# Kernel optimization log

Measured on AMD Instinct MI355X. Metric: run time of the kernel, lower is better.

## Reference

```python
import jax, jax.numpy as jnp
import numpy as np

N_NODES = 50000   # number of graph nodes
N_EDGES = 800000  # avg degree 16
D = 128           # in_dim == all hdims -> residual active every layer
L = 3             # len(cfg['hdims'])


def setup_inputs() -> dict:
    key = jax.random.key(0)
    ks = jax.random.split(key, 8)
    scale = 1.0 / np.sqrt(D)
    x = jax.random.normal(ks[0], (N_NODES, D), dtype=jnp.float32)
    edge_index = jax.random.randint(ks[1], (2, N_EDGES), 0, N_NODES, dtype=jnp.int32)
    in_fc_w = jax.random.normal(ks[2], (D, D), dtype=jnp.float32) * scale
    in_fc_b = jnp.zeros((D,), dtype=jnp.float32)
    # GraphConv per layer: lin_rel (with bias) applied to aggregated neighbors,
    # lin_root (no bias) applied to self features. All layers are DxD -> stack.
    w_rel = jax.random.normal(ks[3], (L, D, D), dtype=jnp.float32) * scale
    b_rel = jnp.zeros((L, D), dtype=jnp.float32)
    w_root = jax.random.normal(ks[4], (L, D, D), dtype=jnp.float32) * scale
    return {"x": x, "edge_index": edge_index, "in_fc_w": in_fc_w,
            "in_fc_b": in_fc_b, "w_rel": w_rel, "b_rel": b_rel, "w_root": w_root}


def reference(x, edge_index, in_fc_w, in_fc_b, w_rel, b_rel, w_root):
    src, dst = edge_index[0], edge_index[1]
    h = x @ in_fc_w + in_fc_b                     # in_fc
    for l in range(L):                            # fixed small layer count
        # GraphConv, aggr='add': gather source feats, scatter-add to targets
        agg = jax.ops.segment_sum(h[src], dst, num_segments=N_NODES)  # [N, D]
        out = agg @ w_rel[l] + b_rel[l] + h @ w_root[l]
        out = jax.nn.relu(out)
        h = out + h                               # residual (dims match)
    return h
```

## Files before the change

kernel.cpp:

```cpp
#include <hip/hip_runtime.h>
#include <hip/hip_bf16.h>


constexpr int D = 128;
constexpr int NB_SHIFT = 7;
constexpr int BCAP = 2560;
constexpr int CHUNK = 2048;

typedef __attribute__((ext_vector_type(8))) short bf16x8;
typedef __attribute__((ext_vector_type(4))) float f32x4;
typedef __attribute__((ext_vector_type(4))) unsigned int u32x4;

__device__ inline unsigned short f2bf(float f) {
    unsigned int u = __builtin_bit_cast(unsigned int, f);
    u += 0x7FFFu + ((u >> 16) & 1u);
    return (unsigned short)(u >> 16);
}
__device__ inline float bf2f(unsigned short v) {
    return __builtin_bit_cast(float, (unsigned int)v << 16);
}
__device__ inline float bf2f_lo(unsigned int v) {
    return __builtin_bit_cast(float, v << 16);
}
__device__ inline float bf2f_hi(unsigned int v) {
    return __builtin_bit_cast(float, v & 0xFFFF0000u);
}

__global__ __launch_bounds__(256) void prep(
    const float* __restrict__ x, const float* __restrict__ fc_w,
    const float* __restrict__ w_rel, const float* __restrict__ w_root,
    unsigned short* __restrict__ xb, unsigned short* __restrict__ Wp,
    int* __restrict__ cursor, int n4, int NB)
{
    int blk = blockIdx.x;
    const int nconv = (n4 + 255) / 256;
    if (blk < nconv) {
        int i = blk * 256 + threadIdx.x;
        if (i < n4) {
            float4 v = ((const float4*)x)[i];
            ushort4 o;
            o.x = f2bf(v.x); o.y = f2bf(v.y); o.z = f2bf(v.z); o.w = f2bf(v.w);
            ((ushort4*)xb)[i] = o;
        }
        return;
    }
    blk -= nconv;
    if (blk < 56) {
        int idx = blk * 256 + threadIdx.x;
        int mat  = idx >> 11;
        int rem  = idx & 2047;
        int tn   = rem >> 8;
        int ks   = (rem >> 6) & 3;
        int lane = rem & 63;
        const float* w = (mat == 0) ? fc_w
                       : (mat <= 3) ? w_rel  + (size_t)(mat - 1) * D * D
                                    : w_root + (size_t)(mat - 4) * D * D;
        unsigned short* wp = Wp + (size_t)mat * D * D + (size_t)rem * 8;
        int kbase = ks * 32 + (lane >> 4) * 8;
        int col   = tn * 16 + (lane & 15);
        #pragma unroll
        for (int j = 0; j < 8; ++j)
            wp[j] = f2bf(w[(size_t)(kbase + j) * D + col]);
        return;
    }
    blk -= 56;
    int i = blk * 256 + threadIdx.x;
    if (i < NB) cursor[i] = 0;
}

__global__ __launch_bounds__(256) void gemm_mfma(
    const unsigned short* __restrict__ A1, const unsigned short* __restrict__ W1p,
    const float* __restrict__ bias, unsigned short* __restrict__ hb_out, int N)
{
    const int tid  = threadIdx.x;
    const int wave = tid >> 6;
    const int lane = tid & 63;
    const int row0 = blockIdx.x * 64 + wave * 16;
    const int mrow = lane & 15;
    const int kgrp = lane >> 4;

    f32x4 acc[8];
    #pragma unroll
    for (int t = 0; t < 8; ++t) acc[t] = (f32x4){0.f, 0.f, 0.f, 0.f};

    int arow = row0 + mrow; if (arow >= N) arow = N - 1;
    const size_t abase = (size_t)arow * D + kgrp * 8;

    #pragma unroll
    for (int ks = 0; ks < 4; ++ks) {
        bf16x8 a1 = *(const bf16x8*)(A1 + abase + ks * 32);
        #pragma unroll
        for (int tn = 0; tn < 8; ++tn) {
            bf16x8 b = *(const bf16x8*)(W1p + ((size_t)((tn * 4 + ks) * 64 + lane) * 8));
            acc[tn] = __builtin_amdgcn_mfma_f32_16x16x32_bf16(a1, b, acc[tn], 0, 0, 0);
        }
    }

    const int r0 = row0 + kgrp * 4;
    #pragma unroll
    for (int tn = 0; tn < 8; ++tn) {
        const int col = tn * 16 + mrow;
        const float bv = bias[col];
        #pragma unroll
        for (int reg = 0; reg < 4; ++reg) {
            int r = r0 + reg;
            if (r < N) hb_out[(size_t)r * D + col] = f2bf(acc[tn][reg] + bv);
        }
    }
}

__global__ __launch_bounds__(256) void gemm_layer(
    const unsigned short* __restrict__ aggb, const unsigned short* __restrict__ hb_in,
    const unsigned short* __restrict__ Wrel, const unsigned short* __restrict__ Wroot,
    const float* __restrict__ bias,
    unsigned short* hb_out, float* out_f32, int N)
{
    const int tid  = threadIdx.x;
    const int wave = tid >> 6;
    const int lane = tid & 63;
    const int row0 = blockIdx.x * 64 + wave * 16;
    const int mrow = lane & 15;
    const int kgrp = lane >> 4;

    f32x4 acc[8];
    #pragma unroll
    for (int t = 0; t < 8; ++t) acc[t] = (f32x4){0.f, 0.f, 0.f, 0.f};

    int arow = row0 + mrow; if (arow >= N) arow = N - 1;
    const size_t abase = (size_t)arow * D + kgrp * 8;

    #pragma unroll
    for (int ks = 0; ks < 4; ++ks) {
        bf16x8 a1 = *(const bf16x8*)(aggb  + abase + ks * 32);
        bf16x8 a2 = *(const bf16x8*)(hb_in + abase + ks * 32);
        #pragma unroll
        for (int tn = 0; tn < 8; ++tn) {
            bf16x8 b1 = *(const bf16x8*)(Wrel  + ((size_t)((tn * 4 + ks) * 64 + lane) * 8));
            acc[tn] = __builtin_amdgcn_mfma_f32_16x16x32_bf16(a1, b1, acc[tn], 0, 0, 0);
            bf16x8 b2 = *(const bf16x8*)(Wroot + ((size_t)((tn * 4 + ks) * 64 + lane) * 8));
            acc[tn] = __builtin_amdgcn_mfma_f32_16x16x32_bf16(a2, b2, acc[tn], 0, 0, 0);
        }
    }

    const int r0 = row0 + kgrp * 4;
    #pragma unroll
    for (int tn = 0; tn < 8; ++tn) {
        const int col = tn * 16 + mrow;
        const float bv = bias[col];
        #pragma unroll
        for (int reg = 0; reg < 4; ++reg) {
            int r = r0 + reg;
            if (r < N) {
                float z = fmaxf(acc[tn][reg] + bv, 0.f);
                float o = z + bf2f(hb_in[(size_t)r * D + col]);
                if (out_f32 != nullptr) out_f32[(size_t)r * D + col] = o;
                else                    hb_out[(size_t)r * D + col] = f2bf(o);
            }
        }
    }
}

__global__ __launch_bounds__(256) void bucket_scatter(
    const int* __restrict__ src, const int* __restrict__ dst,
    unsigned int* __restrict__ entries, int* __restrict__ cursor, int E, int NB)
{
    __shared__ unsigned int   stage[CHUNK];
    __shared__ unsigned short bslot[CHUNK];
    __shared__ int lhist[512];
    __shared__ int lscan[512];
    __shared__ int lgbase[512];
    __shared__ int lcur[512];
    __shared__ int sh[256];

    const int base  = blockIdx.x * CHUNK;
    const int count = min(CHUNK, E - base);
    const int tid   = threadIdx.x;

    for (int i = tid; i < 512; i += 256) { lhist[i] = 0; lcur[i] = 0; }
    __syncthreads();

    for (int i = tid; i < count; i += 256)
        atomicAdd(&lhist[dst[base + i] >> NB_SHIFT], 1);
    __syncthreads();

    int v2 = lhist[2 * tid] + lhist[2 * tid + 1];
    sh[tid] = v2;
    __syncthreads();
    #pragma unroll
    for (int off = 1; off < 256; off <<= 1) {
        int t = (tid >= off) ? sh[tid - off] : 0;
        __syncthreads();
        sh[tid] += t;
        __syncthreads();
    }
    int excl2 = sh[tid] - v2;
    lscan[2 * tid]     = excl2;
    lscan[2 * tid + 1] = excl2 + lhist[2 * tid];
    __syncthreads();

    for (int t = tid; t < 512; t += 256) {
        int c = (t < NB) ? lhist[t] : 0;
        lgbase[t] = (c > 0) ? atomicAdd(&cursor[t], c) : 0;
    }
    __syncthreads();

    for (int i = tid; i < count; i += 256) {
        int d = dst[base + i];
        int s = src[base + i];
        int b = d >> NB_SHIFT;
        int p = atomicAdd(&lcur[b], 1);
        int slot = lscan[b] + p;
        stage[slot] = ((unsigned int)(d & ((1 << NB_SHIFT) - 1)) << 16) | (unsigned int)s;
        bslot[slot] = (unsigned short)b;
    }
    __syncthreads();

    for (int i = tid; i < count; i += 256) {
        int b   = bslot[i];
        int off = i - lscan[b] + lgbase[b];
        if (off < BCAP) entries[(size_t)b * BCAP + off] = stage[i];
    }
}

__global__ __launch_bounds__(256) void bucket_sort(
    const unsigned int* __restrict__ entries, const int* __restrict__ cursor,
    unsigned short* __restrict__ sorted_src, int* __restrict__ rs4,
    int N, int NB, float inv_range)
{
    const int b   = blockIdx.x;
    const int tid = threadIdx.x;

    __shared__ int nhist[512];
    __shared__ int nscan[512];
    __shared__ int ncur[512];
    __shared__ int sh[256];
    __shared__ unsigned short svals[BCAP];
    __shared__ int sgbase;

    int part = 0;
    for (int i = tid; i < b; i += 256) part += min(cursor[i], BCAP);
    sh[tid] = part;
    __syncthreads();
    for (int off = 128; off > 0; off >>= 1) {
        if (tid < off) sh[tid] += sh[tid + off];
        __syncthreads();
    }
    if (tid == 0) sgbase = sh[0];
    const int cnt = min(cursor[b], BCAP);
    __syncthreads();
    const int gbase = sgbase;

    for (int i = tid; i < 512; i += 256) { nhist[i] = 0; ncur[i] = 0; }
    __syncthreads();

    const unsigned int* ebase = entries + (size_t)b * BCAP;
    for (int i = tid; i < cnt; i += 256) {
        unsigned int e = ebase[i];
        int s = (int)(e & 0xFFFFu);
        int r = (int)((float)s * inv_range); if (r > 3) r = 3;
        atomicAdd(&nhist[(int)((e >> 16) << 2) | r], 1);
    }
    __syncthreads();

    int v2 = nhist[2 * tid] + nhist[2 * tid + 1];
    sh[tid] = v2;
    __syncthreads();
    #pragma unroll
    for (int off = 1; off < 256; off <<= 1) {
        int t = (tid >= off) ? sh[tid - off] : 0;
        __syncthreads();
        sh[tid] += t;
        __syncthreads();
    }
    int excl2 = sh[tid] - v2;
    nscan[2 * tid]     = excl2;
    nscan[2 * tid + 1] = excl2 + nhist[2 * tid];
    __syncthreads();

    for (int i = tid; i < 512; i += 256) {
        int n = (b << NB_SHIFT) + (i >> 2);
        if (n < N) rs4[(n << 2) + (i & 3)] = gbase + nscan[i];
    }
    if (b == NB - 1 && tid == 0) rs4[N << 2] = gbase + cnt;

    for (int i = tid; i < cnt; i += 256) {
        unsigned int e = ebase[i];
        int s = (int)(e & 0xFFFFu);
        int r = (int)((float)s * inv_range); if (r > 3) r = 3;
        int key = (int)((e >> 16) << 2) | r;
        int p = atomicAdd(&ncur[key], 1);
        svals[nscan[key] + p] = (unsigned short)s;
    }
    __syncthreads();

    unsigned short* obase = sorted_src + gbase;
    for (int i = tid; i < cnt; i += 256) obase[i] = svals[i];
}

__global__ __launch_bounds__(256) void aggregate_bf16(
    const unsigned short* __restrict__ hb, const int* __restrict__ rs4,
    const unsigned short* __restrict__ sorted_src, unsigned short* __restrict__ aggb, int N)
{
    const int tid  = threadIdx.x;
    const int wave = tid >> 6;
    const int lane = tid & 63;
    const int g    = lane >> 4;
    const int c    = lane & 15;
    const int n    = blockIdx.x * 16 + wave * 4 + g;
    if (n >= N) return;
    const int b = rs4[n << 2];
    const int e = rs4[(n << 2) + 4];

    float acc[8];
    #pragma unroll
    for (int q = 0; q < 8; ++q) acc[q] = 0.f;

    int j = b;
    for (; j + 4 <= e; j += 4) {
        int s0 = sorted_src[j];
        int s1 = sorted_src[j + 1];
        int s2 = sorted_src[j + 2];
        int s3 = sorted_src[j + 3];
        u32x4 v0 = *(const u32x4*)((const unsigned int*)(hb + (size_t)s0 * D) + c * 4);
        u32x4 v1 = *(const u32x4*)((const unsigned int*)(hb + (size_t)s1 * D) + c * 4);
        u32x4 v2 = *(const u32x4*)((const unsigned int*)(hb + (size_t)s2 * D) + c * 4);
        u32x4 v3 = *(const u32x4*)((const unsigned int*)(hb + (size_t)s3 * D) + c * 4);
        #pragma unroll
        for (int q = 0; q < 4; ++q) {
            acc[2 * q]     += (bf2f_lo(v0[q]) + bf2f_lo(v1[q])) + (bf2f_lo(v2[q]) + bf2f_lo(v3[q]));
            acc[2 * q + 1] += (bf2f_hi(v0[q]) + bf2f_hi(v1[q])) + (bf2f_hi(v2[q]) + bf2f_hi(v3[q]));
        }
    }
    for (; j < e; ++j) {
        int s = sorted_src[j];
        u32x4 v = *(const u32x4*)((const unsigned int*)(hb + (size_t)s * D) + c * 4);
        #pragma unroll
        for (int q = 0; q < 4; ++q) {
            acc[2 * q]     += bf2f_lo(v[q]);
            acc[2 * q + 1] += bf2f_hi(v[q]);
        }
    }

    u32x4 o;
    #pragma unroll
    for (int q = 0; q < 4; ++q)
        o[q] = (unsigned int)f2bf(acc[2 * q]) |
               ((unsigned int)f2bf(acc[2 * q + 1]) << 16);
    *(u32x4*)((unsigned int*)(aggb + (size_t)n * D) + c * 4) = o;
}

extern "C" void kernel_launch(void* const* d_in, const int* in_sizes, int n_in,
                              void* d_out, int out_size, void* d_ws, size_t ws_size,
                              hipStream_t stream)
{
    const float* x      = (const float*)d_in[0];
    const int*   ei     = (const int*)  d_in[1];
    const float* fc_w   = (const float*)d_in[2];
    const float* fc_b   = (const float*)d_in[3];
    const float* w_rel  = (const float*)d_in[4];
    const float* b_rel  = (const float*)d_in[5];
    const float* w_root = (const float*)d_in[6];
    float* out = (float*)d_out;

    const int N = in_sizes[0] / D;
    const int E = in_sizes[1] / 2;
    const int* src = ei;
    const int* dst = ei + E;
    const int NB = (N + (1 << NB_SHIFT) - 1) >> NB_SHIFT;

    char* p = (char*)d_ws;
    unsigned short* hb0  = (unsigned short*)p;  p += (size_t)N * D * sizeof(unsigned short);
    unsigned short* hb1  = (unsigned short*)p;  p += (size_t)N * D * sizeof(unsigned short);
    unsigned short* aggb = (unsigned short*)p;  p += (size_t)N * D * sizeof(unsigned short);
    unsigned short* Wp   = (unsigned short*)p;  p += (size_t)7 * D * D * sizeof(unsigned short);
    unsigned int* entries = (unsigned int*)p;   p += (size_t)NB * BCAP * sizeof(unsigned int);
    unsigned short* sorted_src = (unsigned short*)p;  p += (size_t)E * sizeof(unsigned short);
    int* rs4    = (int*)p;                      p += (size_t)(4 * N + 4) * sizeof(int);
    int* cursor = (int*)p;                      p += (size_t)NB * sizeof(int);

    unsigned short* Wp_in   = Wp;
    unsigned short* Wp_rel  = Wp + (size_t)1 * D * D;
    unsigned short* Wp_root = Wp + (size_t)4 * D * D;
    unsigned short* xb = aggb;

    const int n4 = N * D / 4;
    const int gemm_blocks = (N + 63) / 64;
    const int prep_blocks = (n4 + 255) / 256 + 56 + (NB + 255) / 256;

    prep<<<prep_blocks, 256, 0, stream>>>(x, fc_w, w_rel, w_root, xb, Wp, cursor, n4, NB);

    bucket_scatter<<<(E + CHUNK - 1) / CHUNK, 256, 0, stream>>>(
        src, dst, entries, cursor, E, NB);
    bucket_sort<<<NB, 256, 0, stream>>>(
        entries, cursor, sorted_src, rs4, N, NB, 4.0f / (float)N);

    gemm_mfma<<<gemm_blocks, 256, 0, stream>>>(xb, Wp_in, fc_b, hb0, N);

    unsigned short* hin  = hb0;
    unsigned short* hout = hb1;
    for (int l = 0; l < 3; ++l) {
        aggregate_bf16<<<(N + 15) / 16, 256, 0, stream>>>(hin, rs4, sorted_src, aggb, N);
        gemm_layer<<<gemm_blocks, 256, 0, stream>>>(
            aggb, hin,
            Wp_rel + (size_t)l * D * D, Wp_root + (size_t)l * D * D,
            b_rel + (size_t)l * D,
            (l == 2) ? nullptr : hout,
            (l == 2) ? out : nullptr, N);
        unsigned short* t = hin; hin = hout; hout = t;
    }
}
```

Baseline: 269.9 us.

## Fuse neighbor aggregation into the per-layer GEMM via shared-memory tile

Merges the aggregation kernel and the layer GEMM into one kernel per layer. Each 16-node block gathers neighbor sums into an LDS tile, then its four waves each compute two 16-column MFMA output tiles from that tile. This removes the global write and re-read of the aggregated matrix and one launch per layer. The gather loop is also unrolled to 8 edges. In exchange, each block now does only a 16-row GEMM, so the weight matrices are reloaded roughly four times as often. The xb staging buffer is moved onto hb1.

```diff
diff --git a/kernel.cpp b/kernel.cpp
--- a/kernel.cpp
+++ b/kernel.cpp
@@ -109,49 +109,127 @@
     }
 }
 
-__global__ __launch_bounds__(256) void gemm_layer(
-    const unsigned short* __restrict__ aggb, const unsigned short* __restrict__ hb_in,
+__global__ __launch_bounds__(256) void layer_fused(
+    const unsigned short* __restrict__ hb_in, const int* __restrict__ rs4,
+    const unsigned short* __restrict__ sorted_src,
     const unsigned short* __restrict__ Wrel, const unsigned short* __restrict__ Wroot,
     const float* __restrict__ bias,
     unsigned short* hb_out, float* out_f32, int N)
 {
-    const int tid  = threadIdx.x;
-    const int wave = tid >> 6;
-    const int lane = tid & 63;
-    const int row0 = blockIdx.x * 64 + wave * 16;
+    __shared__ unsigned short aggt[16][136];
+
+    const int tid   = threadIdx.x;
+    const int wave  = tid >> 6;
+    const int lane  = tid & 63;
+    const int node0 = blockIdx.x * 16;
+
+    {
+        const int g = lane >> 4;
+        const int c = lane & 15;
+        const int n = node0 + wave * 4 + g;
+
+        float acc[8];
+        #pragma unroll
+        for (int q = 0; q < 8; ++q) acc[q] = 0.f;
+
+        if (n < N) {
+            const int b = rs4[n << 2];
+            const int e = rs4[(n << 2) + 4];
+            int j = b;
+            for (; j + 8 <= e; j += 8) {
+                int s0 = sorted_src[j];
+                int s1 = sorted_src[j + 1];
+                int s2 = sorted_src[j + 2];
+                int s3 = sorted_src[j + 3];
+                int s4 = sorted_src[j + 4];
+                int s5 = sorted_src[j + 5];
+                int s6 = sorted_src[j + 6];
+                int s7 = sorted_src[j + 7];
+                u32x4 v0 = *(const u32x4*)((const unsigned int*)(hb_in + (size_t)s0 * D) + c * 4);
+                u32x4 v1 = *(const u32x4*)((const unsigned int*)(hb_in + (size_t)s1 * D) + c * 4);
+                u32x4 v2 = *(const u32x4*)((const unsigned int*)(hb_in + (size_t)s2 * D) + c * 4);
+                u32x4 v3 = *(const u32x4*)((const unsigned int*)(hb_in + (size_t)s3 * D) + c * 4);
+                u32x4 v4 = *(const u32x4*)((const unsigned int*)(hb_in + (size_t)s4 * D) + c * 4);
+                u32x4 v5 = *(const u32x4*)((const unsigned int*)(hb_in + (size_t)s5 * D) + c * 4);
+                u32x4 v6 = *(const u32x4*)((const unsigned int*)(hb_in + (size_t)s6 * D) + c * 4);
+                u32x4 v7 = *(const u32x4*)((const unsigned int*)(hb_in + (size_t)s7 * D) + c * 4);
+                #pragma unroll
+                for (int q = 0; q < 4; ++q) {
+                    acc[2 * q]     += ((bf2f_lo(v0[q]) + bf2f_lo(v1[q])) + (bf2f_lo(v2[q]) + bf2f_lo(v3[q])))
+                                    + ((bf2f_lo(v4[q]) + bf2f_lo(v5[q])) + (bf2f_lo(v6[q]) + bf2f_lo(v7[q])));
+                    acc[2 * q + 1] += ((bf2f_hi(v0[q]) + bf2f_hi(v1[q])) + (bf2f_hi(v2[q]) + bf2f_hi(v3[q])))
+                                    + ((bf2f_hi(v4[q]) + bf2f_hi(v5[q])) + (bf2f_hi(v6[q]) + bf2f_hi(v7[q])));
+                }
+            }
+            for (; j + 4 <= e; j += 4) {
+                int s0 = sorted_src[j];
+                int s1 = sorted_src[j + 1];
+                int s2 = sorted_src[j + 2];
+                int s3 = sorted_src[j + 3];
+                u32x4 v0 = *(const u32x4*)((const unsigned int*)(hb_in + (size_t)s0 * D) + c * 4);
+                u32x4 v1 = *(const u32x4*)((const unsigned int*)(hb_in + (size_t)s1 * D) + c * 4);
+                u32x4 v2 = *(const u32x4*)((const unsigned int*)(hb_in + (size_t)s2 * D) + c * 4);
+                u32x4 v3 = *(const u32x4*)((const unsigned int*)(hb_in + (size_t)s3 * D) + c * 4);
+                #pragma unroll
+                for (int q = 0; q < 4; ++q) {
+                    acc[2 * q]     += (bf2f_lo(v0[q]) + bf2f_lo(v1[q])) + (bf2f_lo(v2[q]) + bf2f_lo(v3[q]));
+                    acc[2 * q + 1] += (bf2f_hi(v0[q]) + bf2f_hi(v1[q])) + (bf2f_hi(v2[q]) + bf2f_hi(v3[q]));
+                }
+            }
+            for (; j < e; ++j) {
+                int s = sorted_src[j];
+                u32x4 v = *(const u32x4*)((const unsigned int*)(hb_in + (size_t)s * D) + c * 4);
+                #pragma unroll
+                for (int q = 0; q < 4; ++q) {
+                    acc[2 * q]     += bf2f_lo(v[q]);
+                    acc[2 * q + 1] += bf2f_hi(v[q]);
+                }
+            }
+        }
+        u32x4 o;
+        #pragma unroll
+        for (int q = 0; q < 4; ++q)
+            o[q] = (unsigned int)f2bf(acc[2 * q]) |
+                   ((unsigned int)f2bf(acc[2 * q + 1]) << 16);
+        *(u32x4*)&aggt[wave * 4 + g][c * 8] = o;
+    }
+    __syncthreads();
+
     const int mrow = lane & 15;
     const int kgrp = lane >> 4;
 
-    f32x4 acc[8];
-    #pragma unroll
-    for (int t = 0; t < 8; ++t) acc[t] = (f32x4){0.f, 0.f, 0.f, 0.f};
-
-    int arow = row0 + mrow; if (arow >= N) arow = N - 1;
+    f32x4 acc2[2];
+    acc2[0] = (f32x4){0.f, 0.f, 0.f, 0.f};
+    acc2[1] = (f32x4){0.f, 0.f, 0.f, 0.f};
+
+    int arow = node0 + mrow; if (arow >= N) arow = N - 1;
     const size_t abase = (size_t)arow * D + kgrp * 8;
 
     #pragma unroll
     for (int ks = 0; ks < 4; ++ks) {
-        bf16x8 a1 = *(const bf16x8*)(aggb  + abase + ks * 32);
+        bf16x8 a1 = *(const bf16x8*)&aggt[mrow][ks * 32 + kgrp * 8];
         bf16x8 a2 = *(const bf16x8*)(hb_in + abase + ks * 32);
         #pragma unroll
-        for (int tn = 0; tn < 8; ++tn) {
+        for (int t = 0; t < 2; ++t) {
+            const int tn = wave * 2 + t;
             bf16x8 b1 = *(const bf16x8*)(Wrel  + ((size_t)((tn * 4 + ks) * 64 + lane) * 8));
-            acc[tn] = __builtin_amdgcn_mfma_f32_16x16x32_bf16(a1, b1, acc[tn], 0, 0, 0);
+            acc2[t] = __builtin_amdgcn_mfma_f32_16x16x32_bf16(a1, b1, acc2[t], 0, 0, 0);
             bf16x8 b2 = *(const bf16x8*)(Wroot + ((size_t)((tn * 4 + ks) * 64 + lane) * 8));
-            acc[tn] = __builtin_amdgcn_mfma_f32_16x16x32_bf16(a2, b2, acc[tn], 0, 0, 0);
-        }
-    }
-
-    const int r0 = row0 + kgrp * 4;
-    #pragma unroll
-    for (int tn = 0; tn < 8; ++tn) {
+            acc2[t] = __builtin_amdgcn_mfma_f32_16x16x32_bf16(a2, b2, acc2[t], 0, 0, 0);
+        }
+    }
+
+    const int r0 = node0 + kgrp * 4;
+    #pragma unroll
+    for (int t = 0; t < 2; ++t) {
+        const int tn  = wave * 2 + t;
         const int col = tn * 16 + mrow;
         const float bv = bias[col];
         #pragma unroll
         for (int reg = 0; reg < 4; ++reg) {
             int r = r0 + reg;
             if (r < N) {
-                float z = fmaxf(acc[tn][reg] + bv, 0.f);
+                float z = fmaxf(acc2[t][reg] + bv, 0.f);
                 float o = z + bf2f(hb_in[(size_t)r * D + col]);
                 if (out_f32 != nullptr) out_f32[(size_t)r * D + col] = o;
                 else                    hb_out[(size_t)r * D + col] = f2bf(o);
@@ -297,58 +375,6 @@
     for (int i = tid; i < cnt; i += 256) obase[i] = svals[i];
 }
 
-__global__ __launch_bounds__(256) void aggregate_bf16(
-    const unsigned short* __restrict__ hb, const int* __restrict__ rs4,
-    const unsigned short* __restrict__ sorted_src, unsigned short* __restrict__ aggb, int N)
-{
-    const int tid  = threadIdx.x;
-    const int wave = tid >> 6;
-    const int lane = tid & 63;
-    const int g    = lane >> 4;
-    const int c    = lane & 15;
-    const int n    = blockIdx.x * 16 + wave * 4 + g;
-    if (n >= N) return;
-    const int b = rs4[n << 2];
-    const int e = rs4[(n << 2) + 4];
-
-    float acc[8];
-    #pragma unroll
-    for (int q = 0; q < 8; ++q) acc[q] = 0.f;
-
-    int j = b;
-    for (; j + 4 <= e; j += 4) {
-        int s0 = sorted_src[j];
-        int s1 = sorted_src[j + 1];
-        int s2 = sorted_src[j + 2];
-        int s3 = sorted_src[j + 3];
-        u32x4 v0 = *(const u32x4*)((const unsigned int*)(hb + (size_t)s0 * D) + c * 4);
-        u32x4 v1 = *(const u32x4*)((const unsigned int*)(hb + (size_t)s1 * D) + c * 4);
-        u32x4 v2 = *(const u32x4*)((const unsigned int*)(hb + (size_t)s2 * D) + c * 4);
-        u32x4 v3 = *(const u32x4*)((const unsigned int*)(hb + (size_t)s3 * D) + c * 4);
-        #pragma unroll
-        for (int q = 0; q < 4; ++q) {
-            acc[2 * q]     += (bf2f_lo(v0[q]) + bf2f_lo(v1[q])) + (bf2f_lo(v2[q]) + bf2f_lo(v3[q]));
-            acc[2 * q + 1] += (bf2f_hi(v0[q]) + bf2f_hi(v1[q])) + (bf2f_hi(v2[q]) + bf2f_hi(v3[q]));
-        }
-    }
-    for (; j < e; ++j) {
-        int s = sorted_src[j];
-        u32x4 v = *(const u32x4*)((const unsigned int*)(hb + (size_t)s * D) + c * 4);
-        #pragma unroll
-        for (int q = 0; q < 4; ++q) {
-            acc[2 * q]     += bf2f_lo(v[q]);
-            acc[2 * q + 1] += bf2f_hi(v[q]);
-        }
-    }
-
-    u32x4 o;
-    #pragma unroll
-    for (int q = 0; q < 4; ++q)
-        o[q] = (unsigned int)f2bf(acc[2 * q]) |
-               ((unsigned int)f2bf(acc[2 * q + 1]) << 16);
-    *(u32x4*)((unsigned int*)(aggb + (size_t)n * D) + c * 4) = o;
-}
-
 extern "C" void kernel_launch(void* const* d_in, const int* in_sizes, int n_in,
                               void* d_out, int out_size, void* d_ws, size_t ws_size,
                               hipStream_t stream)
@@ -371,7 +397,6 @@
     char* p = (char*)d_ws;
     unsigned short* hb0  = (unsigned short*)p;  p += (size_t)N * D * sizeof(unsigned short);
     unsigned short* hb1  = (unsigned short*)p;  p += (size_t)N * D * sizeof(unsigned short);
-    unsigned short* aggb = (unsigned short*)p;  p += (size_t)N * D * sizeof(unsigned short);
     unsigned short* Wp   = (unsigned short*)p;  p += (size_t)7 * D * D * sizeof(unsigned short);
     unsigned int* entries = (unsigned int*)p;   p += (size_t)NB * BCAP * sizeof(unsigned int);
     unsigned short* sorted_src = (unsigned short*)p;  p += (size_t)E * sizeof(unsigned short);
@@ -381,11 +406,12 @@
     unsigned short* Wp_in   = Wp;
     unsigned short* Wp_rel  = Wp + (size_t)1 * D * D;
     unsigned short* Wp_root = Wp + (size_t)4 * D * D;
-    unsigned short* xb = aggb;
+    unsigned short* xb = hb1;
 
     const int n4 = N * D / 4;
-    const int gemm_blocks = (N + 63) / 64;
-    const int prep_blocks = (n4 + 255) / 256 + 56 + (NB + 255) / 256;
+    const int gemm_blocks  = (N + 63) / 64;
+    const int layer_blocks = (N + 15) / 16;
+    const int prep_blocks  = (n4 + 255) / 256 + 56 + (NB + 255) / 256;
 
     prep<<<prep_blocks, 256, 0, stream>>>(x, fc_w, w_rel, w_root, xb, Wp, cursor, n4, NB);
 
@@ -399,9 +425,8 @@
     unsigned short* hin  = hb0;
     unsigned short* hout = hb1;
     for (int l = 0; l < 3; ++l) {
-        aggregate_bf16<<<(N + 15) / 16, 256, 0, stream>>>(hin, rs4, sorted_src, aggb, N);
-        gemm_layer<<<gemm_blocks, 256, 0, stream>>>(
-            aggb, hin,
+        layer_fused<<<layer_blocks, 256, 0, stream>>>(
+            hin, rs4, sorted_src,
             Wp_rel + (size_t)l * D * D, Wp_root + (size_t)l * D * D,
             b_rel + (size_t)l * D,
             (l == 2) ? nullptr : hout,
```

After: 258.8 us. 4.1% less time.
